# Kernel tuning notes

Measured on AMD Instinct MI355X. Metric: run time of the kernel, lower is better.

Reference implementation:

```python
import jax, jax.numpy as jnp
import numpy as np
from jax.scipy.special import gammaln

BLOCK = 96          # NIQE block size at scale 1 (48 at scale 2)
KSIZE = 7           # gaussian MSCN window size
SIGMA = 7.0 / 6.0   # gaussian sigma
PAD = KSIZE // 2
NUM_FEAT = 18       # features per block per scale

# gamma grid for AGGD shape-parameter search (matches torch.arange(0.2, 10.001, 0.001))
AGGD_GRID = jnp.asarray(np.arange(0.2, 10.0 + 0.001, 0.001), dtype=jnp.float32)
R_GAM = jnp.exp(2.0 * gammaln(2.0 / AGGD_GRID) - (gammaln(1.0 / AGGD_GRID) + gammaln(3.0 / AGGD_GRID)))


def _gauss_kernel():
    m = (KSIZE - 1) / 2.0
    y, x = np.ogrid[-m:m + 1, -m:m + 1]
    h = np.exp(-(x * x + y * y) / (2.0 * SIGMA * SIGMA))
    h[h < np.finfo(h.dtype).eps * h.max()] = 0
    h = h / h.sum()
    return jnp.asarray(h, dtype=jnp.float32)[None, None]  # (1,1,7,7)

GAUSS = _gauss_kernel()


def imfilter(x):
    # replicate ('same') padding + valid conv, like _image_filter
    xp = jnp.pad(x, ((0, 0), (0, 0), (PAD, PAD), (PAD, PAD)), mode='edge')
    return jax.lax.conv_general_dilated(xp, GAUSS, (1, 1), 'VALID')


def estimate_aggd(blocks):
    # blocks: (N, k, k)
    mask_l = blocks < 0
    mask_r = blocks > 0
    cl = jnp.sum(mask_l, axis=(-1, -2)).astype(blocks.dtype)
    cr = jnp.sum(mask_r, axis=(-1, -2)).astype(blocks.dtype)
    left_std = jnp.sqrt(jnp.sum(jnp.where(mask_l, blocks, 0.0) ** 2, axis=(-1, -2)) / (cl + 1e-8))
    right_std = jnp.sqrt(jnp.sum(jnp.where(mask_r, blocks, 0.0) ** 2, axis=(-1, -2)) / (cr + 1e-8))
    gamma_hat = left_std / right_std
    rhat = jnp.mean(jnp.abs(blocks), axis=(-1, -2)) ** 2 / jnp.mean(blocks ** 2, axis=(-1, -2))
    rhat_norm = rhat * (gamma_hat ** 3 + 1.0) * (gamma_hat + 1.0) / (gamma_hat ** 2 + 1.0) ** 2
    pos = jnp.argmin(jnp.abs(R_GAM[None, :] - rhat_norm[:, None]), axis=-1)  # (N, 9801) search
    alpha = AGGD_GRID[pos]
    conv = jnp.sqrt(jnp.exp(gammaln(1.0 / alpha) - gammaln(3.0 / alpha)))
    return alpha, left_std * conv, right_std * conv


def mscn_features(blocks):
    # blocks: (N, k, k) -> (N, 18)
    alpha, lb, rb = estimate_aggd(blocks)
    feats = [alpha, (lb + rb) / 2.0]
    for sh in ((0, 1), (1, 0), (1, 1), (1, -1)):
        shifted = jnp.roll(blocks, sh, axis=(-2, -1))
        a, l, r = estimate_aggd(blocks * shifted)
        mean = (r - l) * jnp.exp(gammaln(2.0 / a) - gammaln(1.0 / a))
        feats.extend((a, mean, l, r))
    return jnp.stack(feats, axis=-1)


def blockify(img, bs):
    # img: (b,1,H,W) -> (b, nb, bs, bs); partial blocks discarded like _blockproc_torch
    b, _, h, w = img.shape
    nbh, nbw = h // bs, w // bs
    x = img[:, 0, :nbh * bs, :nbw * bs].reshape(b, nbh, bs, nbw, bs)
    return x.transpose(0, 1, 3, 2, 4).reshape(b, nbh * nbw, bs, bs)


def mscn_normalize(img):
    mu = imfilter(img)
    sigma = jnp.sqrt(jnp.abs(imfilter(img * img) - mu * mu))
    return (img - mu) / (sigma + 1.0)


def niqe_score(image, mu_pris, cov_pris):
    img = image
    feats = []
    for scale in (1, 2):
        norm = mscn_normalize(img)
        blocks = blockify(norm, BLOCK // scale)
        b, nb, k, _ = blocks.shape
        f = mscn_features(blocks.reshape(b * nb, k, k)).reshape(b, nb, NUM_FEAT)
        feats.append(f)
        if scale == 1:
            # 2x2 average-pool downsample for second scale
            bb, cc, hh, ww = img.shape
            img = img.reshape(bb, cc, hh // 2, 2, ww // 2, 2).mean(axis=(3, 5))
    feats = jnp.concatenate(feats, axis=-1)  # (b, nb, 36)
    nb = feats.shape[1]
    mu_dist = feats.mean(axis=1)                        # (b, 36)
    xm = feats - mu_dist[:, None, :]
    cov_dist = jnp.einsum('bnf,bng->bfg', xm, xm) / (nb - 1)
    cov = (cov_pris[None] + cov_dist) / 2.0
    diff = mu_pris[None, :] - mu_dist                   # (b, 36)
    invc = jnp.linalg.pinv(cov)
    quad = jnp.einsum('bf,bfg,bg->b', diff, invc, diff)
    return jnp.sqrt(jnp.maximum(quad, 0.0))


def setup_inputs() -> dict:
    key = jax.random.key(0)
    k1, k2, k3 = jax.random.split(key, 3)
    image = jax.random.uniform(k1, (16, 1, 1056, 1056), dtype=jnp.float32)
    mu_pris = jax.random.normal(k2, (36,), dtype=jnp.float32)
    a = jax.random.normal(k3, (36, 36), dtype=jnp.float32)
    cov_pris = a @ a.T / 36.0 + 0.5 * jnp.eye(36, dtype=jnp.float32)  # SPD pristine covariance
    return {'image': image, 'mu_pris': mu_pris, 'cov_pris': cov_pris}


def reference(image, mu_pris, cov_pris):
    return niqe_score(image, mu_pris, cov_pris)
```

## Files before the change

### kernel.cpp

```cpp
#include <hip/hip_runtime.h>
#include <math.h>

#define NGRID 9801
#define NB 11
#define NBLK (NB*NB)
#define BATCH 16
#define NFEAT 36

__global__ void init_tables(float* __restrict__ rgam, float* __restrict__ convt,
                            float* __restrict__ meanf, float* __restrict__ w1d) {
    int i = blockIdx.x * blockDim.x + threadIdx.x;
    if (i < NGRID) {
        double a = (double)(float)(0.2 + 0.001 * (double)i);
        double g1 = lgamma(1.0 / a);
        double g2 = lgamma(2.0 / a);
        double g3 = lgamma(3.0 / a);
        rgam[i]  = (float)exp(2.0 * g2 - g1 - g3);
        convt[i] = (float)sqrt(exp(g1 - g3));
        meanf[i] = (float)exp(g2 - g1);
    }
    if (i == 0) {
        double g[7], s = 0.0;
        for (int k = 0; k < 7; ++k) { double d = (double)(k - 3); g[k] = exp(-d * d * 18.0 / 49.0); s += g[k]; }
        for (int k = 0; k < 7; ++k) w1d[k] = (float)(g[k] / s);
    }
}

__device__ __forceinline__ float bperm(int addr, float v) {
    return __int_as_float(__builtin_amdgcn_ds_bpermute(addr, __float_as_int(v)));
}

template <int K, bool WDS>
__global__ __launch_bounds__(256) void fused_mscn_stats(
        const float* __restrict__ img, float* __restrict__ dsout,
        const float* __restrict__ w1d, float* __restrict__ stats) {
    constexpr int NSLAB = K / 48;
    constexpr int NSTRIP = 4 / NSLAB;
    constexpr int SROWS = K / NSTRIP;
    constexpr int W = K * NB;
    constexpr int H = W;

    __shared__ float lastrow[NSTRIP][K];
    __shared__ float edgeL[NSTRIP][NSLAB][SROWS];
    __shared__ float edgeR[NSTRIP][NSLAB][SROWS];
    __shared__ float redf[4][15];
    __shared__ float redc[4][10];

    const int tid = threadIdx.x;
    const int lane = tid & 63;
    const int wv = tid >> 6;
    const int slab = wv % NSLAB;
    const int strip = wv / NSLAB;
    const int bIdx = blockIdx.x;
    const int b = blockIdx.y;
    const int bh = bIdx / NB, bw = bIdx % NB;
    const int x0 = bw * K + slab * 48;
    const int gx = x0 - 3 + lane;
    const int gxc = min(max(gx, 0), W - 1);
    const int r0 = bh * K + strip * SROWS;
    const int basem3 = (lane - 3) << 2;
    const bool act = (lane >= 3) && (lane <= 50);
    int am1, ap1;
    if constexpr (NSLAB == 1) {
        am1 = ((lane == 3) ? 50 : (lane - 1)) << 2;
        ap1 = ((lane == 50) ? 3 : (lane + 1)) << 2;
    } else {
        am1 = ((lane - 1) & 63) << 2;
        ap1 = ((lane + 1) & 63) << 2;
    }

    const float* im = img + (size_t)b * H * W + gxc;
    const float w0=w1d[0], w1=w1d[1], w2=w1d[2], w3=w1d[3], w4=w1d[4], w5=w1d[5], w6=w1d[6];

    auto ld = [&](int r) -> float {
        int rc = min(max(r, 0), H - 1);
        return im[(size_t)rc * W];
    };

    float pa0, pa1, pa2, pa4, pa5, pa6, vHp;
    auto issue_raw = [&](float v) {
        pa0 = bperm(basem3,      v);
        pa1 = bperm(basem3 + 4,  v);
        pa2 = bperm(basem3 + 8,  v);
        pa4 = bperm(basem3 + 16, v);
        pa5 = bperm(basem3 + 20, v);
        pa6 = bperm(basem3 + 24, v);
        vHp = v;
    };
    auto combine_raw = [&](float& om, float& oq) {
        om = ((w0*pa0 + w1*pa1) + (w2*pa2 + w3*vHp)) + ((w4*pa4 + w5*pa5) + w6*pa6);
        oq = ((w0*pa0*pa0 + w1*pa1*pa1) + (w2*pa2*pa2 + w3*vHp*vHp))
           + ((w4*pa4*pa4 + w5*pa5*pa5) + w6*pa6*pa6);
    };

    float acc[5][3];
    #pragma unroll
    for (int s = 0; s < 5; ++s) { acc[s][0] = acc[s][1] = acc[s][2] = 0.f; }
    int cl[5] = {0,0,0,0,0}, cr[5] = {0,0,0,0,0};

    auto upd = [&](int s, float v) {
        float vp = fmaxf(v, 0.f);
        acc[s][0] = fmaf(vp, vp, acc[s][0]);
        acc[s][1] = fmaf(v, v, acc[s][1]);
        acc[s][2] += fabsf(v);
        cl[s] += __popcll(__ballot(v < 0.f));
        cr[s] += __popcll(__ballot(v > 0.f));
    };

    float mr0,mr1,mr2,mr3,mr4,mr5,mr6, qr0,qr1,qr2,qr3,qr4,qr5,qr6;
    float rA, rB, rC, rD;
    float vN = ld(r0 - 3);
    { float v=vN; vN=ld(r0-2); issue_raw(v); combine_raw(mr0,qr0); }
    { float v=vN; vN=ld(r0-1); issue_raw(v); combine_raw(mr1,qr1); }
    { float v=vN; vN=ld(r0+0); issue_raw(v); combine_raw(mr2,qr2); }
    { float v=vN; vN=ld(r0+1); issue_raw(v); combine_raw(mr3,qr3); rA=v; }
    { float v=vN; vN=ld(r0+2); issue_raw(v); combine_raw(mr4,qr4); rB=v; }
    { float v=vN; vN=ld(r0+3); issue_raw(v); combine_raw(mr5,qr5); rC=v; }
    { float v=vN; vN=ld(r0+4); issue_raw(v); combine_raw(mr6,qr6); rD=v; }
    { float v=vN; vN=ld(r0+5); issue_raw(v); }

    float normP = 0.f, normP2 = 0.f;
    float pendSL = 0.f, pendPL = 0.f, pendPR = 0.f;
    float firstN = 0.f, dsSave = 0.f;
    const bool dsw = WDS && (lane & 1) && (lane >= 3) && (lane <= 49);

    #pragma unroll 4
    for (int yy = 0; yy < SROWS; ++yy) {
        const int y = r0 + yy;
        if (yy > 0) {
            upd(0, normP);
            upd(1, normP * pendSL);
            upd(2, normP * normP2);
            upd(3, normP * pendPL);
            upd(4, normP * pendPR);
        }
        float mu = ((w0*mr0 + w1*mr1) + (w2*mr2 + w3*mr3)) + ((w4*mr4 + w5*mr5) + w6*mr6);
        float s2 = ((w0*qr0 + w1*qr1) + (w2*qr2 + w3*qr3)) + ((w4*qr4 + w5*qr5) + w6*qr6);
        float sig = __builtin_amdgcn_sqrtf(fabsf(s2 - mu * mu));
        float nrm = (rA - mu) * __builtin_amdgcn_rcpf(sig + 1.0f);
        float cur = act ? nrm : 0.f;

        if (yy == 0) firstN = cur;
        if constexpr (NSLAB == 2) {
            if (lane == 3)  edgeL[strip][slab][yy] = cur;
            if (lane == 50) edgeR[strip][slab][yy] = cur;
        }
        if (yy == SROWS - 1 && act) lastrow[strip][slab * 48 + lane - 3] = cur;

        if constexpr (WDS) {
            float hs = rA + __shfl_down(rA, 1);
            if ((y & 1) == 0) dsSave = hs;
            else if (dsw)
                dsout[((size_t)b * (H / 2) + (y >> 1)) * (W / 2) + (gx >> 1)] = 0.25f * (dsSave + hs);
        }

        pendSL = bperm(am1, cur);
        pendPL = bperm(am1, normP);
        pendPR = bperm(ap1, normP);
        normP2 = normP; normP = cur;

        float mh, qh; combine_raw(mh, qh);
        mr0=mr1; mr1=mr2; mr2=mr3; mr3=mr4; mr4=mr5; mr5=mr6; mr6=mh;
        qr0=qr1; qr1=qr2; qr2=qr3; qr3=qr4; qr4=qr5; qr5=qr6; qr6=qh;

        rA=rB; rB=rC; rC=rD; rD=vHp;
        float vv = vN; vN = ld(y + 6);
        issue_raw(vv);
    }
    upd(0, normP);
    upd(1, normP * pendSL);
    upd(2, normP * normP2);
    upd(3, normP * pendPL);
    upd(4, normP * pendPR);

    __syncthreads();

    {
        const int ps = (strip + NSTRIP - 1) % NSTRIP;
        int j  = slab * 48 + (lane - 3);
        int js = act ? j : 0;
        int jm1 = (js + K - 1) % K;
        int jp1 = (js + 1) % K;
        float pv  = act ? lastrow[ps][js]  : 0.f;
        float pvL = act ? lastrow[ps][jm1] : 0.f;
        float pvR = act ? lastrow[ps][jp1] : 0.f;
        upd(2, firstN * pv);
        upd(3, firstN * pvL);
        upd(4, firstN * pvR);
    }

    if constexpr (NSLAB == 2) {
        if (lane < SROWS) {
            int r = lane;
            if (slab == 0) {
                float c0  = edgeL[strip][0][r];
                float e95 = edgeR[strip][1][r];
                upd(1, c0 * e95);
                if (r > 0) {
                    upd(3, c0 * edgeR[strip][1][r - 1]);
                    upd(4, edgeR[strip][0][r] * edgeL[strip][1][r - 1]);
                }
            } else {
                float c48 = edgeL[strip][1][r];
                float e47 = edgeR[strip][0][r];
                upd(1, c48 * e47);
                if (r > 0) {
                    upd(3, c48 * edgeR[strip][0][r - 1]);
                    upd(4, edgeR[strip][1][r] * edgeL[strip][0][r - 1]);
                }
            }
        }
    }

    #pragma unroll
    for (int off = 32; off >= 1; off >>= 1)
        #pragma unroll
        for (int s = 0; s < 5; ++s) {
            acc[s][0] += __shfl_down(acc[s][0], off);
            acc[s][1] += __shfl_down(acc[s][1], off);
            acc[s][2] += __shfl_down(acc[s][2], off);
        }
    if (lane == 0) {
        #pragma unroll
        for (int s = 0; s < 5; ++s) {
            redf[wv][s*3+0] = acc[s][0];
            redf[wv][s*3+1] = acc[s][1];
            redf[wv][s*3+2] = acc[s][2];
            redc[wv][s*2+0] = (float)cl[s];
            redc[wv][s*2+1] = (float)cr[s];
        }
    }
    __syncthreads();
    if (tid < 15) {
        stats[((size_t)b * NBLK + bIdx) * 25 + tid] =
            redf[0][tid] + redf[1][tid] + redf[2][tid] + redf[3][tid];
    } else if (tid < 25) {
        int t = tid - 15;
        stats[((size_t)b * NBLK + bIdx) * 25 + tid] =
            redc[0][t] + redc[1][t] + redc[2][t] + redc[3][t];
    }
}

__global__ __launch_bounds__(256) void aggd_kernel(
        const float* __restrict__ stats1, const float* __restrict__ stats2,
        const float* __restrict__ rgam, const float* __restrict__ convt,
        const float* __restrict__ meanf, float* __restrict__ feats) {
    __shared__ float rg[NGRID];
    for (int i = threadIdx.x; i < NGRID; i += 256) rg[i] = rgam[i];
    __syncthreads();

    int gid = blockIdx.x * 256 + threadIdx.x;
    if (gid >= 2 * BATCH * NBLK * 5) return;
    int s = gid % 5; int t = gid / 5;
    int blk = t % NBLK; t /= NBLK;
    int b = t % BATCH; int scale = t / BATCH;

    const float* st = (scale ? stats2 : stats1) + ((size_t)b * NBLK + blk) * 25;
    float sr2 = st[s*3+0], ssq = st[s*3+1], sab = st[s*3+2];
    float cl = st[15 + 2*s], cr = st[15 + 2*s + 1];
    float sl2 = fmaxf(ssq - sr2, 0.f);
    float n = scale ? (48.f * 48.f) : (96.f * 96.f);

    float lstd = sqrtf(sl2 / (cl + 1e-8f));
    float rstd = sqrtf(sr2 / (cr + 1e-8f));
    float gh = lstd / rstd;
    float mab = sab / n;
    float msq = ssq / n;
    float rhat = mab * mab / msq;
    float g2 = gh * gh;
    float x = rhat * (gh * g2 + 1.f) * (gh + 1.f) / ((g2 + 1.f) * (g2 + 1.f));

    int lo = 0, hi = NGRID;
    while (lo < hi) {
        int mid = (lo + hi) >> 1;
        if (rg[mid] < x) lo = mid + 1; else hi = mid;
    }
    int gi;
    if (lo <= 0) gi = 0;
    else if (lo >= NGRID) gi = NGRID - 1;
    else {
        float dlo = x - rg[lo - 1];
        float dhi = rg[lo] - x;
        gi = (dlo <= dhi) ? lo - 1 : lo;
    }

    float alpha = (float)(0.2 + 0.001 * (double)gi);
    float cv = convt[gi];
    float lb = lstd * cv, rb = rstd * cv;
    float* fo = feats + ((size_t)b * NBLK + blk) * NFEAT + (scale ? 18 : 0);
    if (s == 0) {
        fo[0] = alpha;
        fo[1] = 0.5f * (lb + rb);
    } else {
        int o = 2 + (s - 1) * 4;
        fo[o]     = alpha;
        fo[o + 1] = (rb - lb) * meanf[gi];
        fo[o + 2] = lb;
        fo[o + 3] = rb;
    }
}

__global__ __launch_bounds__(256) void score_kernel(
        const float* __restrict__ feats, const float* __restrict__ mu_pris,
        const float* __restrict__ cov_pris, float* __restrict__ out) {
    __shared__ float F[NBLK][NFEAT];
    __shared__ double mu[NFEAT];
    __shared__ double A[NFEAT][NFEAT + 1];
    __shared__ double dff[NFEAT];
    __shared__ double xs[NFEAT];
    int b = blockIdx.x, tid = threadIdx.x;
    const float* fp = feats + (size_t)b * NBLK * NFEAT;
    for (int i = tid; i < NBLK * NFEAT; i += 256) F[i / NFEAT][i % NFEAT] = fp[i];
    __syncthreads();
    if (tid < NFEAT) {
        double s = 0.0;
        for (int n = 0; n < NBLK; ++n) s += (double)F[n][tid];
        mu[tid] = s / (double)NBLK;
        dff[tid] = (double)mu_pris[tid] - mu[tid];
    }
    __syncthreads();
    for (int e = tid; e < NFEAT * NFEAT; e += 256) {
        int f = e / NFEAT, g = e % NFEAT;
        double mf = mu[f], mg = mu[g];
        double s = 0.0;
        for (int n = 0; n < NBLK; ++n) s += ((double)F[n][f] - mf) * ((double)F[n][g] - mg);
        A[f][g] = (s / (double)(NBLK - 1) + (double)cov_pris[f * NFEAT + g]) * 0.5;
    }
    if (tid < NFEAT) A[tid][NFEAT] = dff[tid];
    for (int k = 0; k < NFEAT - 1; ++k) {
        __syncthreads();
        double rk = 1.0 / A[k][k];
        for (int e = tid; e < NFEAT * (NFEAT + 1); e += 256) {
            int r = e / (NFEAT + 1), c = e % (NFEAT + 1);
            if (r > k && c > k) A[r][c] -= (A[r][k] * rk) * A[k][c];
        }
    }
    __syncthreads();
    for (int i = NFEAT - 1; i >= 0; --i) {
        if (tid == i) xs[i] = A[i][NFEAT] / A[i][i];
        __syncthreads();
        if (tid < i) A[tid][NFEAT] -= A[tid][i] * xs[i];
    }
    __syncthreads();
    if (tid == 0) {
        double quad = 0.0;
        for (int i = 0; i < NFEAT; ++i) quad += dff[i] * xs[i];
        out[b] = (float)sqrt(fmax(quad, 0.0));
    }
}

extern "C" void kernel_launch(void* const* d_in, const int* in_sizes, int n_in,
                              void* d_out, int out_size, void* d_ws, size_t ws_size,
                              hipStream_t stream) {
    const float* img      = (const float*)d_in[0];
    const float* mu_pris  = (const float*)d_in[1];
    const float* cov_pris = (const float*)d_in[2];
    float* out = (float*)d_out;
    float* ws = (float*)d_ws;

    float* rgam  = ws;
    float* convt = rgam + 9856;
    float* meanf = convt + 9856;
    float* w1d   = meanf + 9856;
    float* stats1 = w1d + 8;
    float* stats2 = stats1 + BATCH * NBLK * 25;
    float* feats  = stats2 + BATCH * NBLK * 25;
    float* dsimg  = feats + BATCH * NBLK * NFEAT;

    init_tables<<<(NGRID + 255) / 256, 256, 0, stream>>>(rgam, convt, meanf, w1d);

    fused_mscn_stats<96, true><<<dim3(NBLK, BATCH), 256, 0, stream>>>(
        img, dsimg, w1d, stats1);
    fused_mscn_stats<48, false><<<dim3(NBLK, BATCH), 256, 0, stream>>>(
        dsimg, nullptr, w1d, stats2);

    aggd_kernel<<<(2 * BATCH * NBLK * 5 + 255) / 256, 256, 0, stream>>>(
        stats1, stats2, rgam, convt, meanf, feats);

    score_kernel<<<BATCH, 256, 0, stream>>>(feats, mu_pris, cov_pris, out);
}
```

Before: 178.1 us.

## Add dedicated scale-1 kernel with two columns per lane and float2 loads

Replaces the generic templated kernel at scale 1 with a specialized kernel in which each lane handles two adjacent columns. Each wavefront covers the full 96-wide block with 4 row strips, loading rows as float2 and keeping the vertical filter state in register ring buffers. This removes the two-slab edge exchange through shared memory, halves the per-pixel bpermute and ballot work relative to the column count, and fuses the 2x2 downsample write without a shuffle. The generic kernel is simplified to the single-slab path. The cost is higher register pressure from the unrolled ring buffers and more complex boundary handling.

```diff
diff --git a/kernel.cpp b/kernel.cpp
--- a/kernel.cpp
+++ b/kernel.cpp
@@ -30,6 +30,191 @@
     return __int_as_float(__builtin_amdgcn_ds_bpermute(addr, __float_as_int(v)));
 }
 
+__global__ __launch_bounds__(256) void fused96(
+        const float* __restrict__ img, float* __restrict__ dsout,
+        const float* __restrict__ w1d, float* __restrict__ stats) {
+    constexpr int K = 96, W = 1056, H = 1056, SROWS = 24;
+    __shared__ float2 lastrow2[4][48];
+    __shared__ float redf[4][15];
+    __shared__ float redc[4][10];
+
+    const int tid = threadIdx.x;
+    const int lane = tid & 63;
+    const int strip = tid >> 6;
+    const int bIdx = blockIdx.x;
+    const int b = blockIdx.y;
+    const int bh = bIdx / NB, bw = bIdx % NB;
+    const int x0 = bw * K;
+    const int c0 = x0 - 4 + 2 * lane;
+    const int cc = min(max(c0, 0), W - 2);
+    const bool fixL = (c0 < 0), fixR = (c0 >= W);
+    const int r0 = bh * K + strip * SROWS;
+    const bool act = lane < 48;
+
+    const int aP1 = ((lane + 1) & 63) << 2;
+    const int aP2 = ((lane + 2) & 63) << 2;
+    const int aP3 = ((lane + 3) & 63) << 2;
+    const int aP4 = ((lane + 4) & 63) << 2;
+    const int aL = (act ? (lane == 0 ? 47 : lane - 1) : 0) << 2;
+    const int aR = (act ? (lane == 47 ? 0 : lane + 1) : 0) << 2;
+
+    const float* imb = img + (size_t)b * H * W;
+    int roff = max(r0 - 3, 0) * W;
+    int row = r0 - 3;
+    const float w0=w1d[0], w1=w1d[1], w2=w1d[2], w3=w1d[3], w4=w1d[4], w5=w1d[5], w6=w1d[6];
+
+    auto ldrow = [&]() -> float2 {
+        float2 u = *(const float2*)(imb + roff + cc);
+        u.y = fixL ? u.x : u.y;
+        u.x = fixR ? u.y : u.x;
+        roff += (row >= 0 && row < H - 1) ? W : 0;
+        ++row;
+        return u;
+    };
+
+    float ay, bx, by, cx, cy, dx, dy, ex;
+    auto issue_raw = [&](float2 u) {
+        ay = u.y;
+        bx = bperm(aP1, u.x); by = bperm(aP1, u.y);
+        cx = bperm(aP2, u.x); cy = bperm(aP2, u.y);
+        dx = bperm(aP3, u.x); dy = bperm(aP3, u.y);
+        ex = bperm(aP4, u.x);
+    };
+    auto combine_raw = [&](float2& m, float2& q) -> float2 {
+        m.x = ((w0*ay + w1*bx) + (w2*by + w3*cx)) + ((w4*cy + w5*dx) + w6*dy);
+        m.y = ((w0*bx + w1*by) + (w2*cx + w3*cy)) + ((w4*dx + w5*dy) + w6*ex);
+        float say=ay*ay, sbx=bx*bx, sby=by*by, scx=cx*cx, scy=cy*cy, sdx=dx*dx, sdy=dy*dy, sex=ex*ex;
+        q.x = ((w0*say + w1*sbx) + (w2*sby + w3*scx)) + ((w4*scy + w5*sdx) + w6*sdy);
+        q.y = ((w0*sbx + w1*sby) + (w2*scx + w3*scy)) + ((w4*sdx + w5*sdy) + w6*sex);
+        float2 rc; rc.x = cx; rc.y = cy;
+        return rc;
+    };
+
+    float acc[5][3];
+    #pragma unroll
+    for (int s = 0; s < 5; ++s) { acc[s][0] = acc[s][1] = acc[s][2] = 0.f; }
+    int cl[5] = {0,0,0,0,0}, cr[5] = {0,0,0,0,0};
+    auto upd2 = [&](int s, float vx, float vy) {
+        float px = fmaxf(vx, 0.f), py = fmaxf(vy, 0.f);
+        acc[s][0] = fmaf(px, px, fmaf(py, py, acc[s][0]));
+        acc[s][1] = fmaf(vx, vx, fmaf(vy, vy, acc[s][1]));
+        acc[s][2] += fabsf(vx) + fabsf(vy);
+        cl[s] += __popcll(__ballot(vx < 0.f)) + __popcll(__ballot(vy < 0.f));
+        cr[s] += __popcll(__ballot(vx > 0.f)) + __popcll(__ballot(vy > 0.f));
+    };
+
+    float2 m2[8], q2[8], rawc[8];
+    #pragma unroll
+    for (int t = -3; t <= 3; ++t) {
+        float2 u = ldrow();
+        issue_raw(u);
+        float2 rc = combine_raw(m2[(t + 3) & 7], q2[(t + 3) & 7]);
+        if (t >= 0) rawc[t & 7] = rc;
+    }
+    { float2 u = ldrow(); issue_raw(u); }
+    float2 vn0 = ldrow();
+    float2 vn1 = ldrow();
+
+    float2 prev; prev.x = prev.y = 0.f;
+    float2 prev2; prev2.x = prev2.y = 0.f;
+    float pendSL = 0.f, pendPL = 0.f, pendPR = 0.f;
+    float2 firstN; firstN.x = firstN.y = 0.f;
+    float dsSave = 0.f;
+    float* dsp = dsout + ((size_t)b * (H / 2) + (r0 >> 1)) * (W / 2) + (bw * 48 + (act ? lane : 0));
+
+    auto do_stats = [&]() {
+        upd2(0, prev.x, prev.y);
+        upd2(1, prev.x * pendSL,  prev.y * prev.x);
+        upd2(2, prev.x * prev2.x, prev.y * prev2.y);
+        upd2(3, prev.x * pendPL,  prev.y * prev2.x);
+        upd2(4, prev.x * prev2.y, prev.y * pendPR);
+    };
+
+    #pragma unroll 1
+    for (int yo = 0; yo < 3; ++yo) {
+        #pragma unroll
+        for (int c = 0; c < 8; ++c) {
+            if (c > 0) { do_stats(); }
+            else if (yo > 0) { do_stats(); }
+
+            float mux = ((w0*m2[c&7].x + w1*m2[(c+1)&7].x) + (w2*m2[(c+2)&7].x + w3*m2[(c+3)&7].x))
+                      + ((w4*m2[(c+4)&7].x + w5*m2[(c+5)&7].x) + w6*m2[(c+6)&7].x);
+            float muy = ((w0*m2[c&7].y + w1*m2[(c+1)&7].y) + (w2*m2[(c+2)&7].y + w3*m2[(c+3)&7].y))
+                      + ((w4*m2[(c+4)&7].y + w5*m2[(c+5)&7].y) + w6*m2[(c+6)&7].y);
+            float s2x = ((w0*q2[c&7].x + w1*q2[(c+1)&7].x) + (w2*q2[(c+2)&7].x + w3*q2[(c+3)&7].x))
+                      + ((w4*q2[(c+4)&7].x + w5*q2[(c+5)&7].x) + w6*q2[(c+6)&7].x);
+            float s2y = ((w0*q2[c&7].y + w1*q2[(c+1)&7].y) + (w2*q2[(c+2)&7].y + w3*q2[(c+3)&7].y))
+                      + ((w4*q2[(c+4)&7].y + w5*q2[(c+5)&7].y) + w6*q2[(c+6)&7].y);
+            float2 rA = rawc[c & 7];
+            float nx = (rA.x - mux) * __builtin_amdgcn_rcpf(__builtin_amdgcn_sqrtf(fabsf(s2x - mux*mux)) + 1.0f);
+            float ny = (rA.y - muy) * __builtin_amdgcn_rcpf(__builtin_amdgcn_sqrtf(fabsf(s2y - muy*muy)) + 1.0f);
+            float2 cur; cur.x = act ? nx : 0.f; cur.y = act ? ny : 0.f;
+
+            if (c == 0 && yo == 0) firstN = cur;
+            if (c == 7 && yo == 2 && act) lastrow2[strip][lane] = cur;
+
+            float hs = rA.x + rA.y;
+            if ((c & 1) == 0) { dsSave = hs; }
+            else {
+                if (act) *dsp = 0.25f * (dsSave + hs);
+                dsp += (W / 2);
+            }
+
+            pendSL = bperm(aL, cur.y);
+            pendPL = bperm(aL, prev.y);
+            pendPR = bperm(aR, prev.x);
+            prev2 = prev; prev = cur;
+
+            rawc[(c + 4) & 7] = combine_raw(m2[(c + 7) & 7], q2[(c + 7) & 7]);
+
+            if ((c & 1) == 0) { float2 t = vn0; vn0 = ldrow(); issue_raw(t); }
+            else              { float2 t = vn1; vn1 = ldrow(); issue_raw(t); }
+        }
+    }
+    do_stats();
+
+    __syncthreads();
+
+    if (act) {
+        const int ps = (strip + 3) & 3;
+        float2 pv  = lastrow2[ps][lane];
+        float2 lft = lastrow2[ps][lane == 0 ? 47 : lane - 1];
+        float2 rgt = lastrow2[ps][lane == 47 ? 0 : lane + 1];
+        upd2(2, firstN.x * pv.x,  firstN.y * pv.y);
+        upd2(3, firstN.x * lft.y, firstN.y * pv.x);
+        upd2(4, firstN.x * pv.y,  firstN.y * rgt.x);
+    }
+
+    #pragma unroll
+    for (int off = 32; off >= 1; off >>= 1)
+        #pragma unroll
+        for (int s = 0; s < 5; ++s) {
+            acc[s][0] += __shfl_down(acc[s][0], off);
+            acc[s][1] += __shfl_down(acc[s][1], off);
+            acc[s][2] += __shfl_down(acc[s][2], off);
+        }
+    const int wv = strip;
+    if (lane == 0) {
+        #pragma unroll
+        for (int s = 0; s < 5; ++s) {
+            redf[wv][s*3+0] = acc[s][0];
+            redf[wv][s*3+1] = acc[s][1];
+            redf[wv][s*3+2] = acc[s][2];
+            redc[wv][s*2+0] = (float)cl[s];
+            redc[wv][s*2+1] = (float)cr[s];
+        }
+    }
+    __syncthreads();
+    if (tid < 15) {
+        stats[((size_t)b * NBLK + bIdx) * 25 + tid] =
+            redf[0][tid] + redf[1][tid] + redf[2][tid] + redf[3][tid];
+    } else if (tid < 25) {
+        int t = tid - 15;
+        stats[((size_t)b * NBLK + bIdx) * 25 + tid] =
+            redc[0][t] + redc[1][t] + redc[2][t] + redc[3][t];
+    }
+}
+
 template <int K, bool WDS>
 __global__ __launch_bounds__(256) void fused_mscn_stats(
         const float* __restrict__ img, float* __restrict__ dsout,
@@ -41,8 +226,6 @@
     constexpr int H = W;
 
     __shared__ float lastrow[NSTRIP][K];
-    __shared__ float edgeL[NSTRIP][NSLAB][SROWS];
-    __shared__ float edgeR[NSTRIP][NSLAB][SROWS];
     __shared__ float redf[4][15];
     __shared__ float redc[4][10];
 
@@ -60,14 +243,8 @@
     const int r0 = bh * K + strip * SROWS;
     const int basem3 = (lane - 3) << 2;
     const bool act = (lane >= 3) && (lane <= 50);
-    int am1, ap1;
-    if constexpr (NSLAB == 1) {
-        am1 = ((lane == 3) ? 50 : (lane - 1)) << 2;
-        ap1 = ((lane == 50) ? 3 : (lane + 1)) << 2;
-    } else {
-        am1 = ((lane - 1) & 63) << 2;
-        ap1 = ((lane + 1) & 63) << 2;
-    }
+    int am1 = ((lane == 3) ? 50 : (lane - 1)) << 2;
+    int ap1 = ((lane == 50) ? 3 : (lane + 1)) << 2;
 
     const float* im = img + (size_t)b * H * W + gxc;
     const float w0=w1d[0], w1=w1d[1], w2=w1d[2], w3=w1d[3], w4=w1d[4], w5=w1d[5], w6=w1d[6];
@@ -121,8 +298,7 @@
 
     float normP = 0.f, normP2 = 0.f;
     float pendSL = 0.f, pendPL = 0.f, pendPR = 0.f;
-    float firstN = 0.f, dsSave = 0.f;
-    const bool dsw = WDS && (lane & 1) && (lane >= 3) && (lane <= 49);
+    float firstN = 0.f;
 
     #pragma unroll 4
     for (int yy = 0; yy < SROWS; ++yy) {
@@ -141,18 +317,7 @@
         float cur = act ? nrm : 0.f;
 
         if (yy == 0) firstN = cur;
-        if constexpr (NSLAB == 2) {
-            if (lane == 3)  edgeL[strip][slab][yy] = cur;
-            if (lane == 50) edgeR[strip][slab][yy] = cur;
-        }
         if (yy == SROWS - 1 && act) lastrow[strip][slab * 48 + lane - 3] = cur;
-
-        if constexpr (WDS) {
-            float hs = rA + __shfl_down(rA, 1);
-            if ((y & 1) == 0) dsSave = hs;
-            else if (dsw)
-                dsout[((size_t)b * (H / 2) + (y >> 1)) * (W / 2) + (gx >> 1)] = 0.25f * (dsSave + hs);
-        }
 
         pendSL = bperm(am1, cur);
         pendPL = bperm(am1, normP);
@@ -187,29 +352,6 @@
         upd(2, firstN * pv);
         upd(3, firstN * pvL);
         upd(4, firstN * pvR);
-    }
-
-    if constexpr (NSLAB == 2) {
-        if (lane < SROWS) {
-            int r = lane;
-            if (slab == 0) {
-                float c0  = edgeL[strip][0][r];
-                float e95 = edgeR[strip][1][r];
-                upd(1, c0 * e95);
-                if (r > 0) {
-                    upd(3, c0 * edgeR[strip][1][r - 1]);
-                    upd(4, edgeR[strip][0][r] * edgeL[strip][1][r - 1]);
-                }
-            } else {
-                float c48 = edgeL[strip][1][r];
-                float e47 = edgeR[strip][0][r];
-                upd(1, c48 * e47);
-                if (r > 0) {
-                    upd(3, c48 * edgeR[strip][0][r - 1]);
-                    upd(4, edgeR[strip][1][r] * edgeL[strip][0][r - 1]);
-                }
-            }
-        }
     }
 
     #pragma unroll
@@ -369,8 +511,7 @@
 
     init_tables<<<(NGRID + 255) / 256, 256, 0, stream>>>(rgam, convt, meanf, w1d);
 
-    fused_mscn_stats<96, true><<<dim3(NBLK, BATCH), 256, 0, stream>>>(
-        img, dsimg, w1d, stats1);
+    fused96<<<dim3(NBLK, BATCH), 256, 0, stream>>>(img, dsimg, w1d, stats1);
     fused_mscn_stats<48, false><<<dim3(NBLK, BATCH), 256, 0, stream>>>(
         dsimg, nullptr, w1d, stats2);
 
```

Measured after the change: 196.4 us. +10.3%, slower.

## Use 8 waves for scale-1 MSCN stats and reuse neighbor permutes across rows

Applied to the files above, without the earlier changes.

For the 96-pixel scale, each block now runs 4 row strips × 2 slabs (512 threads) instead of 2 strips, which halves the rows per wave and doubles parallelism across the 1936 blocks. The per-row permutes are cut from three to two by keeping the left/right neighbor values of the current row and using the previous row's copies for the diagonal products. Row addressing is also made incremental, and the unroll factor rises to 6. The cost is more strip-boundary fixups and reductions, plus possible register-pressure effects from the larger block.

```diff
diff --git a/kernel.cpp b/kernel.cpp
--- a/kernel.cpp
+++ b/kernel.cpp
@@ -31,11 +31,12 @@
 }
 
 template <int K, bool WDS>
-__global__ __launch_bounds__(256) void fused_mscn_stats(
+__global__ __launch_bounds__(K == 96 ? 512 : 256) void fused_mscn_stats(
         const float* __restrict__ img, float* __restrict__ dsout,
         const float* __restrict__ w1d, float* __restrict__ stats) {
     constexpr int NSLAB = K / 48;
-    constexpr int NSTRIP = 4 / NSLAB;
+    constexpr int NSTRIP = 4;
+    constexpr int WAVES = NSLAB * NSTRIP;
     constexpr int SROWS = K / NSTRIP;
     constexpr int W = K * NB;
     constexpr int H = W;
@@ -43,8 +44,8 @@
     __shared__ float lastrow[NSTRIP][K];
     __shared__ float edgeL[NSTRIP][NSLAB][SROWS];
     __shared__ float edgeR[NSTRIP][NSLAB][SROWS];
-    __shared__ float redf[4][15];
-    __shared__ float redc[4][10];
+    __shared__ float redf[WAVES][15];
+    __shared__ float redc[WAVES][10];
 
     const int tid = threadIdx.x;
     const int lane = tid & 63;
@@ -69,12 +70,16 @@
         ap1 = ((lane + 1) & 63) << 2;
     }
 
-    const float* im = img + (size_t)b * H * W + gxc;
+    const float* imb = img + (size_t)b * H * W;
     const float w0=w1d[0], w1=w1d[1], w2=w1d[2], w3=w1d[3], w4=w1d[4], w5=w1d[5], w6=w1d[6];
 
-    auto ld = [&](int r) -> float {
-        int rc = min(max(r, 0), H - 1);
-        return im[(size_t)rc * W];
+    int row = r0 - 3;
+    int roff = min(max(row, 0), H - 1) * W;
+    auto ld = [&]() -> float {
+        float v = imb[(size_t)(roff + gxc)];
+        ++row;
+        roff = min(max(row, 0), H - 1) * W;
+        return v;
     };
 
     float pa0, pa1, pa2, pa4, pa5, pa6, vHp;
@@ -109,30 +114,30 @@
 
     float mr0,mr1,mr2,mr3,mr4,mr5,mr6, qr0,qr1,qr2,qr3,qr4,qr5,qr6;
     float rA, rB, rC, rD;
-    float vN = ld(r0 - 3);
-    { float v=vN; vN=ld(r0-2); issue_raw(v); combine_raw(mr0,qr0); }
-    { float v=vN; vN=ld(r0-1); issue_raw(v); combine_raw(mr1,qr1); }
-    { float v=vN; vN=ld(r0+0); issue_raw(v); combine_raw(mr2,qr2); }
-    { float v=vN; vN=ld(r0+1); issue_raw(v); combine_raw(mr3,qr3); rA=v; }
-    { float v=vN; vN=ld(r0+2); issue_raw(v); combine_raw(mr4,qr4); rB=v; }
-    { float v=vN; vN=ld(r0+3); issue_raw(v); combine_raw(mr5,qr5); rC=v; }
-    { float v=vN; vN=ld(r0+4); issue_raw(v); combine_raw(mr6,qr6); rD=v; }
-    { float v=vN; vN=ld(r0+5); issue_raw(v); }
-
+    float vN = ld();
+    { float v=vN; vN=ld(); issue_raw(v); combine_raw(mr0,qr0); }
+    { float v=vN; vN=ld(); issue_raw(v); combine_raw(mr1,qr1); }
+    { float v=vN; vN=ld(); issue_raw(v); combine_raw(mr2,qr2); }
+    { float v=vN; vN=ld(); issue_raw(v); combine_raw(mr3,qr3); rA=v; }
+    { float v=vN; vN=ld(); issue_raw(v); combine_raw(mr4,qr4); rB=v; }
+    { float v=vN; vN=ld(); issue_raw(v); combine_raw(mr5,qr5); rC=v; }
+    { float v=vN; vN=ld(); issue_raw(v); combine_raw(mr6,qr6); rD=v; }
+    { float v=vN; vN=ld(); issue_raw(v); }
+
+    float SLa = 0.f, SLb = 0.f, SRa = 0.f, SRb = 0.f;
     float normP = 0.f, normP2 = 0.f;
-    float pendSL = 0.f, pendPL = 0.f, pendPR = 0.f;
     float firstN = 0.f, dsSave = 0.f;
     const bool dsw = WDS && (lane & 1) && (lane >= 3) && (lane <= 49);
 
-    #pragma unroll 4
+    #pragma unroll 6
     for (int yy = 0; yy < SROWS; ++yy) {
         const int y = r0 + yy;
         if (yy > 0) {
             upd(0, normP);
-            upd(1, normP * pendSL);
+            upd(1, normP * SLa);
             upd(2, normP * normP2);
-            upd(3, normP * pendPL);
-            upd(4, normP * pendPR);
+            upd(3, normP * SLb);
+            upd(4, normP * SRb);
         }
         float mu = ((w0*mr0 + w1*mr1) + (w2*mr2 + w3*mr3)) + ((w4*mr4 + w5*mr5) + w6*mr6);
         float s2 = ((w0*qr0 + w1*qr1) + (w2*qr2 + w3*qr3)) + ((w4*qr4 + w5*qr5) + w6*qr6);
@@ -154,9 +159,9 @@
                 dsout[((size_t)b * (H / 2) + (y >> 1)) * (W / 2) + (gx >> 1)] = 0.25f * (dsSave + hs);
         }
 
-        pendSL = bperm(am1, cur);
-        pendPL = bperm(am1, normP);
-        pendPR = bperm(ap1, normP);
+        SLb = SLa; SRb = SRa;
+        SLa = bperm(am1, cur);
+        SRa = bperm(ap1, cur);
         normP2 = normP; normP = cur;
 
         float mh, qh; combine_raw(mh, qh);
@@ -164,14 +169,14 @@
         qr0=qr1; qr1=qr2; qr2=qr3; qr3=qr4; qr4=qr5; qr5=qr6; qr6=qh;
 
         rA=rB; rB=rC; rC=rD; rD=vHp;
-        float vv = vN; vN = ld(y + 6);
+        float vv = vN; vN = ld();
         issue_raw(vv);
     }
     upd(0, normP);
-    upd(1, normP * pendSL);
+    upd(1, normP * SLa);
     upd(2, normP * normP2);
-    upd(3, normP * pendPL);
-    upd(4, normP * pendPR);
+    upd(3, normP * SLb);
+    upd(4, normP * SRb);
 
     __syncthreads();
 
@@ -232,12 +237,16 @@
     }
     __syncthreads();
     if (tid < 15) {
-        stats[((size_t)b * NBLK + bIdx) * 25 + tid] =
-            redf[0][tid] + redf[1][tid] + redf[2][tid] + redf[3][tid];
+        float s = 0.f;
+        #pragma unroll
+        for (int w = 0; w < WAVES; ++w) s += redf[w][tid];
+        stats[((size_t)b * NBLK + bIdx) * 25 + tid] = s;
     } else if (tid < 25) {
         int t = tid - 15;
-        stats[((size_t)b * NBLK + bIdx) * 25 + tid] =
-            redc[0][t] + redc[1][t] + redc[2][t] + redc[3][t];
+        float s = 0.f;
+        #pragma unroll
+        for (int w = 0; w < WAVES; ++w) s += redc[w][t];
+        stats[((size_t)b * NBLK + bIdx) * 25 + tid] = s;
     }
 }
 
@@ -369,7 +378,7 @@
 
     init_tables<<<(NGRID + 255) / 256, 256, 0, stream>>>(rgam, convt, meanf, w1d);
 
-    fused_mscn_stats<96, true><<<dim3(NBLK, BATCH), 256, 0, stream>>>(
+    fused_mscn_stats<96, true><<<dim3(NBLK, BATCH), 512, 0, stream>>>(
         img, dsimg, w1d, stats1);
     fused_mscn_stats<48, false><<<dim3(NBLK, BATCH), 256, 0, stream>>>(
         dsimg, nullptr, w1d, stats2);
```

After: 257.8 us. 44.8% more time.

## Derive product sign counts from ballot masks and deepen row prefetch

Applied to the files above, without the earlier changes.

The change removes the ten ballots per row that counted signs of the pairwise products. It now takes two ballots of the current normalized value and derives the product sign counts with XOR, AND and popcount on 64-bit masks, rotating the masks to handle the horizontal neighbours. Row loads switch to an incrementing byte offset with edge clamping in place of per-row min/max and multiply. A second prefetched row is kept to hide more load latency. The cost is extra scalar bit work and some register pressure, and the rotation logic for the single-slab case has to be correct.

```diff
diff --git a/kernel.cpp b/kernel.cpp
--- a/kernel.cpp
+++ b/kernel.cpp
@@ -69,12 +69,16 @@
         ap1 = ((lane + 1) & 63) << 2;
     }
 
-    const float* im = img + (size_t)b * H * W + gxc;
+    const char* baseB = (const char*)(img + (size_t)b * H * W);
     const float w0=w1d[0], w1=w1d[1], w2=w1d[2], w3=w1d[3], w4=w1d[4], w5=w1d[5], w6=w1d[6];
 
-    auto ld = [&](int r) -> float {
-        int rc = min(max(r, 0), H - 1);
-        return im[(size_t)rc * W];
+    int addrB = (min(max(r0 - 3, 0), H - 1) * W + gxc) * 4;
+    int rowNext = r0 - 2;
+    auto ld = [&]() -> float {
+        float v = *(const float*)(baseB + addrB);
+        addrB += (rowNext >= 1 && rowNext < H) ? (W * 4) : 0;
+        ++rowNext;
+        return v;
     };
 
     float pa0, pa1, pa2, pa4, pa5, pa6, vHp;
@@ -106,18 +110,52 @@
         cl[s] += __popcll(__ballot(v < 0.f));
         cr[s] += __popcll(__ballot(v > 0.f));
     };
+    auto updv = [&](int s, float v) {
+        float vp = fmaxf(v, 0.f);
+        acc[s][0] = fmaf(vp, vp, acc[s][0]);
+        acc[s][1] = fmaf(v, v, acc[s][1]);
+        acc[s][2] += fabsf(v);
+    };
+
+    unsigned long long mA = 0, pA = 0, nzA = 0, mB = 0, nzB = 0;
+    auto shl1 = [&](unsigned long long x) -> unsigned long long {
+        if constexpr (NSLAB == 1) {
+            unsigned long long w = (x >> 3) & 0xFFFFFFFFFFFFULL;
+            w = ((w << 1) | (w >> 47)) & 0xFFFFFFFFFFFFULL;
+            return w << 3;
+        } else return x << 1;
+    };
+    auto shr1 = [&](unsigned long long x) -> unsigned long long {
+        if constexpr (NSLAB == 1) {
+            unsigned long long w = (x >> 3) & 0xFFFFFFFFFFFFULL;
+            w = ((w >> 1) | (w << 47)) & 0xFFFFFFFFFFFFULL;
+            return w << 3;
+        } else return x >> 1;
+    };
+    auto count_row = [&]() {
+        cl[0] += __popcll(mA); cr[0] += __popcll(pA);
+        { unsigned long long x = mA ^ shl1(mA), v = nzA & shl1(nzA);
+          int n = __popcll(x & v); cl[1] += n; cr[1] += __popcll(v) - n; }
+        { unsigned long long x = mA ^ mB, v = nzA & nzB;
+          int n = __popcll(x & v); cl[2] += n; cr[2] += __popcll(v) - n; }
+        { unsigned long long x = mA ^ shl1(mB), v = nzA & shl1(nzB);
+          int n = __popcll(x & v); cl[3] += n; cr[3] += __popcll(v) - n; }
+        { unsigned long long x = mA ^ shr1(mB), v = nzA & shr1(nzB);
+          int n = __popcll(x & v); cl[4] += n; cr[4] += __popcll(v) - n; }
+    };
 
     float mr0,mr1,mr2,mr3,mr4,mr5,mr6, qr0,qr1,qr2,qr3,qr4,qr5,qr6;
     float rA, rB, rC, rD;
-    float vN = ld(r0 - 3);
-    { float v=vN; vN=ld(r0-2); issue_raw(v); combine_raw(mr0,qr0); }
-    { float v=vN; vN=ld(r0-1); issue_raw(v); combine_raw(mr1,qr1); }
-    { float v=vN; vN=ld(r0+0); issue_raw(v); combine_raw(mr2,qr2); }
-    { float v=vN; vN=ld(r0+1); issue_raw(v); combine_raw(mr3,qr3); rA=v; }
-    { float v=vN; vN=ld(r0+2); issue_raw(v); combine_raw(mr4,qr4); rB=v; }
-    { float v=vN; vN=ld(r0+3); issue_raw(v); combine_raw(mr5,qr5); rC=v; }
-    { float v=vN; vN=ld(r0+4); issue_raw(v); combine_raw(mr6,qr6); rD=v; }
-    { float v=vN; vN=ld(r0+5); issue_raw(v); }
+    float vN = ld();
+    { float v=vN; vN=ld(); issue_raw(v); combine_raw(mr0,qr0); }
+    { float v=vN; vN=ld(); issue_raw(v); combine_raw(mr1,qr1); }
+    { float v=vN; vN=ld(); issue_raw(v); combine_raw(mr2,qr2); }
+    { float v=vN; vN=ld(); issue_raw(v); combine_raw(mr3,qr3); rA=v; }
+    { float v=vN; vN=ld(); issue_raw(v); combine_raw(mr4,qr4); rB=v; }
+    { float v=vN; vN=ld(); issue_raw(v); combine_raw(mr5,qr5); rC=v; }
+    { float v=vN; vN=ld(); issue_raw(v); combine_raw(mr6,qr6); rD=v; }
+    { float v=vN; vN=ld(); issue_raw(v); }
+    float vN2 = ld();
 
     float normP = 0.f, normP2 = 0.f;
     float pendSL = 0.f, pendPL = 0.f, pendPR = 0.f;
@@ -128,11 +166,12 @@
     for (int yy = 0; yy < SROWS; ++yy) {
         const int y = r0 + yy;
         if (yy > 0) {
-            upd(0, normP);
-            upd(1, normP * pendSL);
-            upd(2, normP * normP2);
-            upd(3, normP * pendPL);
-            upd(4, normP * pendPR);
+            updv(0, normP);
+            updv(1, normP * pendSL);
+            updv(2, normP * normP2);
+            updv(3, normP * pendPL);
+            updv(4, normP * pendPR);
+            count_row();
         }
         float mu = ((w0*mr0 + w1*mr1) + (w2*mr2 + w3*mr3)) + ((w4*mr4 + w5*mr5) + w6*mr6);
         float s2 = ((w0*qr0 + w1*qr1) + (w2*qr2 + w3*qr3)) + ((w4*qr4 + w5*qr5) + w6*qr6);
@@ -158,20 +197,25 @@
         pendPL = bperm(am1, normP);
         pendPR = bperm(ap1, normP);
         normP2 = normP; normP = cur;
+        mB = mA; nzB = nzA;
+        mA = __ballot(cur < 0.f);
+        pA = __ballot(cur > 0.f);
+        nzA = mA | pA;
 
         float mh, qh; combine_raw(mh, qh);
         mr0=mr1; mr1=mr2; mr2=mr3; mr3=mr4; mr4=mr5; mr5=mr6; mr6=mh;
         qr0=qr1; qr1=qr2; qr2=qr3; qr3=qr4; qr4=qr5; qr5=qr6; qr6=qh;
 
         rA=rB; rB=rC; rC=rD; rD=vHp;
-        float vv = vN; vN = ld(y + 6);
+        float vv = vN; vN = vN2; vN2 = ld();
         issue_raw(vv);
     }
-    upd(0, normP);
-    upd(1, normP * pendSL);
-    upd(2, normP * normP2);
-    upd(3, normP * pendPL);
-    upd(4, normP * pendPR);
+    updv(0, normP);
+    updv(1, normP * pendSL);
+    updv(2, normP * normP2);
+    updv(3, normP * pendPL);
+    updv(4, normP * pendPR);
+    count_row();
 
     __syncthreads();
 
```

Result: faster. 174.3 us (-2.1%).
